# Performance work log

Measured on AMD Instinct MI355X. Metric: run time of the kernel, lower is better.

## Reference

```python
import jax, jax.numpy as jnp
import numpy as np

D_MODEL = 1024
NUM_HEADS = 16
D_K = D_MODEL // NUM_HEADS
B, S = 4, 2048


def setup_inputs() -> dict:
    key = jax.random.key(0)
    ks = jax.random.split(key, 11)
    scale = 1.0 / np.sqrt(D_MODEL)
    inp = {
        'query': jax.random.normal(ks[0], (B, S, D_MODEL), dtype=jnp.float32),
        'key':   jax.random.normal(ks[1], (B, S, D_MODEL), dtype=jnp.float32),
        'value': jax.random.normal(ks[2], (B, S, D_MODEL), dtype=jnp.float32),
        'Wq': jax.random.normal(ks[3], (D_MODEL, D_MODEL), dtype=jnp.float32) * scale,
        'bq': jnp.zeros((D_MODEL,), dtype=jnp.float32),
        'Wk': jax.random.normal(ks[4], (D_MODEL, D_MODEL), dtype=jnp.float32) * scale,
        'bk': jnp.zeros((D_MODEL,), dtype=jnp.float32),
        'Wv': jax.random.normal(ks[5], (D_MODEL, D_MODEL), dtype=jnp.float32) * scale,
        'bv': jnp.zeros((D_MODEL,), dtype=jnp.float32),
        'Wo': jax.random.normal(ks[6], (D_MODEL, D_MODEL), dtype=jnp.float32) * scale,
        'bo': jnp.zeros((D_MODEL,), dtype=jnp.float32),
    }
    return inp


def reference(query, key, value, Wq, bq, Wk, bk, Wv, bv, Wo, bo):
    b, sq, _ = query.shape
    sk = key.shape[1]
    # projections (torch Linear: x @ W.T + b; here W stored as [in, out])
    Q = query @ Wq + bq
    K = key @ Wk + bk
    V = value @ Wv + bv
    # split heads: [b, h, s, d_k]
    Q = Q.reshape(b, sq, NUM_HEADS, D_K).transpose(0, 2, 1, 3)
    K = K.reshape(b, sk, NUM_HEADS, D_K).transpose(0, 2, 1, 3)
    V = V.reshape(b, sk, NUM_HEADS, D_K).transpose(0, 2, 1, 3)
    # scaled dot-product attention (full [b,h,sq,sk] scores, as in source)
    scores = jnp.einsum('bhqd,bhkd->bhqk', Q, K) / jnp.sqrt(jnp.float32(D_K))
    attn = jax.nn.softmax(scores, axis=-1)
    out = jnp.einsum('bhqk,bhkd->bhqd', attn, V)
    out = out.transpose(0, 2, 1, 3).reshape(b, sq, D_MODEL)
    return out @ Wo + bo
```

## Files before the change

### kernel.cpp

```cpp
#include <hip/hip_runtime.h>
#include <hip/hip_bf16.h>
#include <stdint.h>

typedef __bf16 bf16x8 __attribute__((ext_vector_type(8)));
typedef __bf16 bf16x4 __attribute__((ext_vector_type(4)));
typedef float  f32x4  __attribute__((ext_vector_type(4)));
typedef unsigned short u16;

#define D_MODEL 1024
#define NUM_HEADS 16
#define DK 64
#define BATCH 4
#define SEQ 2048
#define M_TOTAL (BATCH*SEQ)
#define MD ((size_t)M_TOTAL * D_MODEL)
#define QK_SCALE 0.18033688011112042f

static __device__ __forceinline__ u16 f2bf(float f) {
    __bf16 h = (__bf16)f;
    return __builtin_bit_cast(u16, h);
}

#define ASYNC16(gptr, lptr) __builtin_amdgcn_global_load_lds( \
    (const __attribute__((address_space(1))) unsigned*)(uintptr_t)(gptr), \
    (__attribute__((address_space(3))) unsigned*)(unsigned)(uintptr_t)(lptr), 16, 0, 0)

__global__ void detect_dtype(const u16* __restrict__ q, unsigned* __restrict__ flag) {
    __shared__ int sh[256];
    int cnt = 0;
    for (int i = threadIdx.x; i < 8192; i += 256) {
        u16 v = q[2 * i];
        int e = (v >> 7) & 0xFF;
        if (e >= 100 && e <= 134) cnt++;
    }
    sh[threadIdx.x] = cnt;
    __syncthreads();
    for (int s = 128; s > 0; s >>= 1) {
        if (threadIdx.x < s) sh[threadIdx.x] += sh[threadIdx.x + s];
        __syncthreads();
    }
    if (threadIdx.x == 0) *flag = (sh[0] > 4096) ? 1u : 0u;
}

__global__ __launch_bounds__(256) void convert_bf16(
    const u16* __restrict__ q, const u16* __restrict__ k, const u16* __restrict__ v,
    u16* __restrict__ CVT, const unsigned* __restrict__ flagp)
{
    if (*flagp != 0) return;
    const int z = blockIdx.y;
    const float* src = (const float*)((z == 0) ? q : (z == 1) ? k : v);
    u16* dst = CVT + (size_t)z * MD;
    const size_t stride = (size_t)gridDim.x * 256 * 8;
    for (size_t base = ((size_t)blockIdx.x * 256 + threadIdx.x) * 8; base < MD; base += stride) {
        float4 f0 = *(const float4*)(src + base);
        float4 f1 = *(const float4*)(src + base + 4);
        bf16x8 p;
        p[0] = (__bf16)f0.x; p[1] = (__bf16)f0.y; p[2] = (__bf16)f0.z; p[3] = (__bf16)f0.w;
        p[4] = (__bf16)f1.x; p[5] = (__bf16)f1.y; p[6] = (__bf16)f1.z; p[7] = (__bf16)f1.w;
        *(bf16x8*)(dst + base) = p;
    }
}

__global__ void transpose_w(const u16* __restrict__ W0, const u16* __restrict__ W1,
                            const u16* __restrict__ W2, const u16* __restrict__ W3,
                            u16* __restrict__ WT, const unsigned* __restrict__ flagp) {
    __shared__ u16 tile[32][33];
    const u16* W = (blockIdx.z == 0) ? W0 : (blockIdx.z == 1) ? W1 : (blockIdx.z == 2) ? W2 : W3;
    u16* T = WT + (size_t)blockIdx.z * D_MODEL * D_MODEL;
    bool is_bf16 = (*flagp != 0);
    int x = threadIdx.x, y0 = threadIdx.y;
    int bx = blockIdx.x * 32, by = blockIdx.y * 32;
    if (is_bf16) {
#pragma unroll
        for (int i = 0; i < 4; i++) {
            int y = y0 + i * 8;
            tile[y][x] = W[(size_t)(by + y) * D_MODEL + bx + x];
        }
    } else {
        const float* Wf = (const float*)W;
#pragma unroll
        for (int i = 0; i < 4; i++) {
            int y = y0 + i * 8;
            tile[y][x] = f2bf(Wf[(size_t)(by + y) * D_MODEL + bx + x]);
        }
    }
    __syncthreads();
#pragma unroll
    for (int i = 0; i < 4; i++) {
        int y = y0 + i * 8;
        T[(size_t)(bx + y) * D_MODEL + by + x] = tile[x][y];
    }
}

__global__ __launch_bounds__(256) void gemm_qkv(
    const u16* __restrict__ qin, const u16* __restrict__ kin, const u16* __restrict__ vin,
    const u16* __restrict__ CVT, const u16* __restrict__ WT,
    const u16* __restrict__ bq, const u16* __restrict__ bk, const u16* __restrict__ bv,
    u16* __restrict__ Qp, u16* __restrict__ Kp, u16* __restrict__ VpT,
    const unsigned* __restrict__ flagp)
{
    __shared__ __align__(16) u16 As[128 * 64];
    __shared__ __align__(16) u16 Bs[128 * 64];

    const int id  = blockIdx.x;
    const int wg  = (id & 7) * 192 + (id >> 3);
    const int z   = wg >> 9;
    const int rr  = wg & 511;
    const int m_blk = (rr >> 3) * 128;
    const int n_blk = (rr & 7) * 128;

    const bool is_bf16 = (*flagp != 0);
    const u16* A = is_bf16 ? ((z == 0) ? qin : (z == 1) ? kin : vin)
                           : (CVT + (size_t)z * MD);
    const u16* W    = WT + (size_t)z * 1048576;
    const u16* bias = (z == 0) ? bq : (z == 1) ? bk : bv;
    u16* C          = (z == 0) ? Qp : (z == 1) ? Kp : VpT;
    const float oscale = (z == 0) ? QK_SCALE : 1.0f;

    const int tid  = threadIdx.x;
    const int lane = tid & 63, w = tid >> 6;
    const int quad = lane >> 4, l15 = lane & 15;
    const int swz  = l15 & 7;
    const int wm = w >> 1, wn = w & 1;

    const int lrow = lane >> 3;
    const int ug   = (lane & 7) ^ lrow;

    f32x4 acc[4][4] = {};

    for (int k0 = 0; k0 < D_MODEL; k0 += 64) {
#pragma unroll
        for (int i = 0; i < 4; i++) {
            const int c = w * 4 + i;
            ASYNC16(A + (size_t)(m_blk + c * 8 + lrow) * D_MODEL + k0 + ug * 8, &As[c * 512]);
            ASYNC16(W + (size_t)(n_blk + c * 8 + lrow) * D_MODEL + k0 + ug * 8, &Bs[c * 512]);
        }
        __syncthreads();

        bf16x8 a[4][2], b[4][2];
#pragma unroll
        for (int mf = 0; mf < 4; mf++)
#pragma unroll
            for (int ks = 0; ks < 2; ks++)
                a[mf][ks] = *(const bf16x8*)&As[(size_t)(wm * 64 + mf * 16 + l15) * 64
                                                + (((ks * 4 + quad) ^ swz) * 8)];
#pragma unroll
        for (int nf = 0; nf < 4; nf++)
#pragma unroll
            for (int ks = 0; ks < 2; ks++)
                b[nf][ks] = *(const bf16x8*)&Bs[(size_t)(wn * 64 + nf * 16 + l15) * 64
                                                + (((ks * 4 + quad) ^ swz) * 8)];
#pragma unroll
        for (int mf = 0; mf < 4; mf++)
#pragma unroll
            for (int nf = 0; nf < 4; nf++)
#pragma unroll
                for (int ks = 0; ks < 2; ks++)
                    acc[mf][nf] = __builtin_amdgcn_mfma_f32_16x16x32_bf16(
                        a[mf][ks], b[nf][ks], acc[mf][nf], 0, 0, 0);
        __syncthreads();
    }

#pragma unroll
    for (int nf = 0; nf < 4; nf++) {
        const int n = n_blk + wn * 64 + nf * 16 + l15;
        const float bvf = is_bf16 ? (float)((const __bf16*)bias)[n] : ((const float*)bias)[n];
#pragma unroll
        for (int mf = 0; mf < 4; mf++) {
            const int mrow = m_blk + wm * 64 + mf * 16 + quad * 4;
            if (z == 2) {
                const int bb = mrow >> 11, s = mrow & 2047;
                ushort4 pk;
                pk.x = f2bf(acc[mf][nf][0] + bvf);
                pk.y = f2bf(acc[mf][nf][1] + bvf);
                pk.z = f2bf(acc[mf][nf][2] + bvf);
                pk.w = f2bf(acc[mf][nf][3] + bvf);
                *(ushort4*)(C + (size_t)bb * D_MODEL * SEQ + (size_t)n * SEQ + s) = pk;
            } else {
#pragma unroll
                for (int r = 0; r < 4; r++)
                    C[(size_t)(mrow + r) * D_MODEL + n] = f2bf((acc[mf][nf][r] + bvf) * oscale);
            }
        }
    }
}

__global__ __launch_bounds__(256) void gemm_o(
    const u16* __restrict__ A, const u16* __restrict__ WT,
    const u16* __restrict__ bias, u16* __restrict__ C,
    const unsigned* __restrict__ flagp)
{
    __shared__ __align__(16) u16 As[64 * 32];
    __shared__ __align__(16) u16 Bs[128 * 32];
    const int id  = blockIdx.x;
    const int xcd = id & 7, j = id >> 3;
    const int by  = xcd * 16 + (j >> 3);
    const int bx  = j & 7;

    const int tid  = threadIdx.x;
    const int lane = tid & 63, w = tid >> 6;
    const int quad = lane >> 4, l15 = lane & 15;
    const int wm = w >> 1, wn = w & 1;
    const int m_blk = by * 64, n_blk = bx * 128;
    const bool is_bf16 = (*flagp != 0);

    f32x4 acc[2][4] = {};
    const int srow = lane >> 2, skp = (lane & 3) * 8;

    for (int k0 = 0; k0 < D_MODEL; k0 += 32) {
#pragma unroll
        for (int i = 0; i < 3; i++) {
            int c = w * 3 + i;
            if (c < 4)
                ASYNC16(A  + (size_t)(m_blk + c * 16 + srow) * D_MODEL + k0 + skp, &As[c * 512]);
            else
                ASYNC16(WT + (size_t)(n_blk + (c - 4) * 16 + srow) * D_MODEL + k0 + skp, &Bs[(c - 4) * 512]);
        }
        __syncthreads();

        bf16x8 af[2], bg[4];
#pragma unroll
        for (int sm = 0; sm < 2; sm++)
            af[sm] = *(const bf16x8*)&As[(wm * 32 + sm * 16 + l15) * 32 + quad * 8];
#pragma unroll
        for (int sn = 0; sn < 4; sn++)
            bg[sn] = *(const bf16x8*)&Bs[(wn * 64 + sn * 16 + l15) * 32 + quad * 8];
#pragma unroll
        for (int sm = 0; sm < 2; sm++)
#pragma unroll
            for (int sn = 0; sn < 4; sn++)
                acc[sm][sn] = __builtin_amdgcn_mfma_f32_16x16x32_bf16(af[sm], bg[sn], acc[sm][sn], 0, 0, 0);
        __syncthreads();
    }

#pragma unroll
    for (int sn = 0; sn < 4; sn++) {
        int n = n_blk + wn * 64 + sn * 16 + l15;
        float bvf = is_bf16 ? (float)((const __bf16*)bias)[n] : ((const float*)bias)[n];
#pragma unroll
        for (int sm = 0; sm < 2; sm++) {
            int mrow = m_blk + wm * 32 + sm * 16 + quad * 4;
            if (!is_bf16) {
                float* Cf = (float*)C;
#pragma unroll
                for (int r = 0; r < 4; r++)
                    Cf[(size_t)(mrow + r) * D_MODEL + n] = acc[sm][sn][r] + bvf;
            } else {
#pragma unroll
                for (int r = 0; r < 4; r++)
                    C[(size_t)(mrow + r) * D_MODEL + n] = f2bf(acc[sm][sn][r] + bvf);
            }
        }
    }
}

__global__ __launch_bounds__(256) void attn_kernel(
    const u16* __restrict__ Qp, const u16* __restrict__ Kp,
    const u16* __restrict__ VpT, u16* __restrict__ AO)
{
    __shared__ __align__(16) u16 Ks[2][64 * 64];
    __shared__ __align__(16) u16 Vs[2][64 * 64];
    __shared__ __align__(16) u16 Ps[4][32][68];
    const int id  = blockIdx.x;
    const int xcd = id & 7, j = id >> 3;
    const int bh  = xcd * 8 + (j >> 4);
    const int qx  = j & 15;

    const int tid  = threadIdx.x;
    const int lane = tid & 63, w = tid >> 6;
    const int quad = lane >> 4, l15 = lane & 15;
    const int b = bh >> 4, h = bh & 15;
    const int q_base = qx * 128 + w * 32;

    bf16x8 bQ[2][2];
#pragma unroll
    for (int sn = 0; sn < 2; sn++)
#pragma unroll
        for (int ds = 0; ds < 2; ds++)
            bQ[sn][ds] = *(const bf16x8*)(Qp + (size_t)(b * SEQ + q_base + sn * 16 + l15) * D_MODEL
                                              + h * DK + ds * 32 + quad * 8);

    float lsum[2] = {0.0f, 0.0f};
    f32x4 OT[2][4] = {};

    const u16* Kbase = Kp  + (size_t)(b * SEQ) * D_MODEL + h * DK;
    const u16* Vbase = VpT + (size_t)b * D_MODEL * SEQ + (size_t)(h * DK) * SEQ;

    const int c0   = w * 2;
    const int lrow = lane >> 3;
    const int ug   = (lane & 7) ^ lrow;
    const int swz  = l15 & 7;

    auto issue_tile = [&](int key0, int bf) {
#pragma unroll
        for (int i = 0; i < 2; i++) {
            int c = c0 + i;
            ASYNC16(Kbase + (size_t)(key0 + c * 8 + lrow) * D_MODEL + ug * 8, &Ks[bf][c * 512]);
            ASYNC16(Vbase + (size_t)(c * 8 + lrow) * SEQ + key0 + ug * 8,     &Vs[bf][c * 512]);
        }
    };

    issue_tile(0, 0);
    __syncthreads();

    for (int t = 0; t < SEQ / 64; t++) {
        const int cur = t & 1;
        if (t + 1 < SEQ / 64) issue_tile((t + 1) * 64, cur ^ 1);

#pragma unroll
        for (int kc = 0; kc < 4; kc++) {
            const int krow = (kc * 16 + l15) * 64;
            bf16x8 k0 = *(const bf16x8*)&Ks[cur][krow + ((quad ^ swz) * 8)];
            bf16x8 k1 = *(const bf16x8*)&Ks[cur][krow + (((4 + quad) ^ swz) * 8)];
#pragma unroll
            for (int sn = 0; sn < 2; sn++) {
                f32x4 s = {};
                s = __builtin_amdgcn_mfma_f32_16x16x32_bf16(k0, bQ[sn][0], s, 0, 0, 0);
                s = __builtin_amdgcn_mfma_f32_16x16x32_bf16(k1, bQ[sn][1], s, 0, 0, 0);
                float p0 = __builtin_amdgcn_exp2f(s[0]);
                float p1 = __builtin_amdgcn_exp2f(s[1]);
                float p2 = __builtin_amdgcn_exp2f(s[2]);
                float p3 = __builtin_amdgcn_exp2f(s[3]);
                lsum[sn] += (p0 + p1) + (p2 + p3);
                bf16x4 pk;
                pk[0] = (__bf16)p0; pk[1] = (__bf16)p1; pk[2] = (__bf16)p2; pk[3] = (__bf16)p3;
                *(bf16x4*)&Ps[w][sn * 16 + l15][kc * 16 + quad * 4] = pk;
            }
        }

#pragma unroll
        for (int kc2 = 0; kc2 < 2; kc2++) {
            bf16x8 bP0 = *(const bf16x8*)&Ps[w][l15][kc2 * 32 + quad * 8];
            bf16x8 bP1 = *(const bf16x8*)&Ps[w][16 + l15][kc2 * 32 + quad * 8];
#pragma unroll
            for (int nd = 0; nd < 4; nd++) {
                bf16x8 aV = *(const bf16x8*)&Vs[cur][(nd * 16 + l15) * 64
                                                    + (((kc2 * 4 + quad) ^ swz) * 8)];
                OT[0][nd] = __builtin_amdgcn_mfma_f32_16x16x32_bf16(aV, bP0, OT[0][nd], 0, 0, 0);
                OT[1][nd] = __builtin_amdgcn_mfma_f32_16x16x32_bf16(aV, bP1, OT[1][nd], 0, 0, 0);
            }
        }
        __syncthreads();
    }

#pragma unroll
    for (int sn = 0; sn < 2; sn++) {
        lsum[sn] += __shfl_xor(lsum[sn], 16, 64);
        lsum[sn] += __shfl_xor(lsum[sn], 32, 64);
        float rl = 1.0f / lsum[sn];
        size_t rowbase = (size_t)(b * SEQ + q_base + sn * 16 + l15) * D_MODEL + h * DK;
#pragma unroll
        for (int nd = 0; nd < 4; nd++) {
            ushort4 pk;
            pk.x = f2bf(OT[sn][nd][0] * rl);
            pk.y = f2bf(OT[sn][nd][1] * rl);
            pk.z = f2bf(OT[sn][nd][2] * rl);
            pk.w = f2bf(OT[sn][nd][3] * rl);
            *(ushort4*)(AO + rowbase + nd * 16 + quad * 4) = pk;
        }
    }
}

extern "C" void kernel_launch(void* const* d_in, const int* in_sizes, int n_in,
                              void* d_out, int out_size, void* d_ws, size_t ws_size,
                              hipStream_t stream) {
    const u16* q  = (const u16*)d_in[0];
    const u16* k  = (const u16*)d_in[1];
    const u16* v  = (const u16*)d_in[2];
    const u16* Wq = (const u16*)d_in[3];
    const u16* bq = (const u16*)d_in[4];
    const u16* Wk = (const u16*)d_in[5];
    const u16* bk = (const u16*)d_in[6];
    const u16* Wv = (const u16*)d_in[7];
    const u16* bv = (const u16*)d_in[8];
    const u16* Wo = (const u16*)d_in[9];
    const u16* bo = (const u16*)d_in[10];

    u16* ws   = (u16*)d_ws;
    unsigned* flagp = (unsigned*)ws;
    u16* WT   = ws + 16;
    u16* Qp   = WT + (size_t)4 * 1024 * 1024;
    u16* Kp   = Qp + MD;
    u16* VpT  = Kp + MD;
    u16* CVT  = VpT + MD;
    u16* AO   = CVT;

    detect_dtype<<<1, 256, 0, stream>>>(q, flagp);
    convert_bf16<<<dim3(1024, 3), 256, 0, stream>>>(q, k, v, CVT, flagp);
    transpose_w<<<dim3(32, 32, 4), dim3(32, 8), 0, stream>>>(Wq, Wk, Wv, Wo, WT, flagp);
    gemm_qkv<<<1536, 256, 0, stream>>>(q, k, v, CVT, WT, bq, bk, bv, Qp, Kp, VpT, flagp);
    attn_kernel<<<1024, 256, 0, stream>>>(Qp, Kp, VpT, AO);
    gemm_o<<<1024, 256, 0, stream>>>(AO, WT + 3 * 1048576, bo, (u16*)d_out, flagp);
}
```

Baseline: 400.4 us.

## Double attention block size to 8 waves and compute row sums via MFMA

The attention kernel now launches 512-thread blocks covering 256 queries each, so every K/V tile loaded into shared memory is reused by eight waves instead of four, and each wave issues a single async load per tile. The softmax denominator is now produced by an extra MFMA against a ones vector over the bf16 probabilities, replacing per-lane exp accumulation and the cross-lane shuffles. This halves the K/V global traffic per query and removes VALU adds, at the cost of two extra MFMAs per sub-tile, a larger P buffer in shared memory, and a row sum taken from bf16-rounded probabilities.

```diff
diff --git a/kernel.cpp b/kernel.cpp
--- a/kernel.cpp
+++ b/kernel.cpp
@@ -254,23 +254,23 @@
     }
 }
 
-__global__ __launch_bounds__(256) void attn_kernel(
+__global__ __launch_bounds__(512, 4) void attn_kernel(
     const u16* __restrict__ Qp, const u16* __restrict__ Kp,
     const u16* __restrict__ VpT, u16* __restrict__ AO)
 {
     __shared__ __align__(16) u16 Ks[2][64 * 64];
     __shared__ __align__(16) u16 Vs[2][64 * 64];
-    __shared__ __align__(16) u16 Ps[4][32][68];
+    __shared__ __align__(16) u16 Ps[8][32][68];
     const int id  = blockIdx.x;
     const int xcd = id & 7, j = id >> 3;
-    const int bh  = xcd * 8 + (j >> 4);
-    const int qx  = j & 15;
+    const int bh  = xcd * 8 + (j >> 3);
+    const int qx  = j & 7;
 
     const int tid  = threadIdx.x;
     const int lane = tid & 63, w = tid >> 6;
     const int quad = lane >> 4, l15 = lane & 15;
     const int b = bh >> 4, h = bh & 15;
-    const int q_base = qx * 128 + w * 32;
+    const int q_base = qx * 256 + w * 32;
 
     bf16x8 bQ[2][2];
 #pragma unroll
@@ -280,24 +280,22 @@
             bQ[sn][ds] = *(const bf16x8*)(Qp + (size_t)(b * SEQ + q_base + sn * 16 + l15) * D_MODEL
                                               + h * DK + ds * 32 + quad * 8);
 
-    float lsum[2] = {0.0f, 0.0f};
     f32x4 OT[2][4] = {};
+    f32x4 OTs[2]  = {};
+    bf16x8 aOnes;
+#pragma unroll
+    for (int i = 0; i < 8; i++) aOnes[i] = (__bf16)1.0f;
 
     const u16* Kbase = Kp  + (size_t)(b * SEQ) * D_MODEL + h * DK;
     const u16* Vbase = VpT + (size_t)b * D_MODEL * SEQ + (size_t)(h * DK) * SEQ;
 
-    const int c0   = w * 2;
     const int lrow = lane >> 3;
     const int ug   = (lane & 7) ^ lrow;
     const int swz  = l15 & 7;
 
     auto issue_tile = [&](int key0, int bf) {
-#pragma unroll
-        for (int i = 0; i < 2; i++) {
-            int c = c0 + i;
-            ASYNC16(Kbase + (size_t)(key0 + c * 8 + lrow) * D_MODEL + ug * 8, &Ks[bf][c * 512]);
-            ASYNC16(Vbase + (size_t)(c * 8 + lrow) * SEQ + key0 + ug * 8,     &Vs[bf][c * 512]);
-        }
+        ASYNC16(Kbase + (size_t)(key0 + w * 8 + lrow) * D_MODEL + ug * 8, &Ks[bf][w * 512]);
+        ASYNC16(Vbase + (size_t)(w * 8 + lrow) * SEQ + key0 + ug * 8,     &Vs[bf][w * 512]);
     };
 
     issue_tile(0, 0);
@@ -317,13 +315,11 @@
                 f32x4 s = {};
                 s = __builtin_amdgcn_mfma_f32_16x16x32_bf16(k0, bQ[sn][0], s, 0, 0, 0);
                 s = __builtin_amdgcn_mfma_f32_16x16x32_bf16(k1, bQ[sn][1], s, 0, 0, 0);
-                float p0 = __builtin_amdgcn_exp2f(s[0]);
-                float p1 = __builtin_amdgcn_exp2f(s[1]);
-                float p2 = __builtin_amdgcn_exp2f(s[2]);
-                float p3 = __builtin_amdgcn_exp2f(s[3]);
-                lsum[sn] += (p0 + p1) + (p2 + p3);
                 bf16x4 pk;
-                pk[0] = (__bf16)p0; pk[1] = (__bf16)p1; pk[2] = (__bf16)p2; pk[3] = (__bf16)p3;
+                pk[0] = (__bf16)__builtin_amdgcn_exp2f(s[0]);
+                pk[1] = (__bf16)__builtin_amdgcn_exp2f(s[1]);
+                pk[2] = (__bf16)__builtin_amdgcn_exp2f(s[2]);
+                pk[3] = (__bf16)__builtin_amdgcn_exp2f(s[3]);
                 *(bf16x4*)&Ps[w][sn * 16 + l15][kc * 16 + quad * 4] = pk;
             }
         }
@@ -332,6 +328,8 @@
         for (int kc2 = 0; kc2 < 2; kc2++) {
             bf16x8 bP0 = *(const bf16x8*)&Ps[w][l15][kc2 * 32 + quad * 8];
             bf16x8 bP1 = *(const bf16x8*)&Ps[w][16 + l15][kc2 * 32 + quad * 8];
+            OTs[0] = __builtin_amdgcn_mfma_f32_16x16x32_bf16(aOnes, bP0, OTs[0], 0, 0, 0);
+            OTs[1] = __builtin_amdgcn_mfma_f32_16x16x32_bf16(aOnes, bP1, OTs[1], 0, 0, 0);
 #pragma unroll
             for (int nd = 0; nd < 4; nd++) {
                 bf16x8 aV = *(const bf16x8*)&Vs[cur][(nd * 16 + l15) * 64
@@ -345,9 +343,7 @@
 
 #pragma unroll
     for (int sn = 0; sn < 2; sn++) {
-        lsum[sn] += __shfl_xor(lsum[sn], 16, 64);
-        lsum[sn] += __shfl_xor(lsum[sn], 32, 64);
-        float rl = 1.0f / lsum[sn];
+        float rl = 1.0f / OTs[sn][0];
         size_t rowbase = (size_t)(b * SEQ + q_base + sn * 16 + l15) * D_MODEL + h * DK;
 #pragma unroll
         for (int nd = 0; nd < 4; nd++) {
@@ -389,6 +385,6 @@
     convert_bf16<<<dim3(1024, 3), 256, 0, stream>>>(q, k, v, CVT, flagp);
     transpose_w<<<dim3(32, 32, 4), dim3(32, 8), 0, stream>>>(Wq, Wk, Wv, Wo, WT, flagp);
     gemm_qkv<<<1536, 256, 0, stream>>>(q, k, v, CVT, WT, bq, bk, bv, Qp, Kp, VpT, flagp);
-    attn_kernel<<<1024, 256, 0, stream>>>(Qp, Kp, VpT, AO);
+    attn_kernel<<<512, 512, 0, stream>>>(Qp, Kp, VpT, AO);
     gemm_o<<<1024, 256, 0, stream>>>(AO, WT + 3 * 1048576, bo, (u16*)d_out, flagp);
 }
```

New measurement: 381.7 us. -4.7%, faster.
